# Kernel optimization log

Measured on AMD Instinct MI355X. Metric: run time of the kernel, lower is better.

The kernel has to match this reference:

```python
import jax, jax.numpy as jnp
import numpy as np

D_MODEL = 512
N_HEAD = 8
D_HEAD = D_MODEL // N_HEAD
NEG_INF = -1e30


def _rel_shift(x):
    # x: [b, h, i, j]  -- Transformer-XL relative shift trick
    b, h, i, j = x.shape
    x = jnp.pad(x, ((0, 0), (0, 0), (0, 0), (1, 0)))  # pad left on last dim
    x = x.reshape(b, h, j + 1, i)[:, :, 1:, :]
    return x.reshape(b, h, i, j)


def setup_inputs() -> dict:
    key = jax.random.key(0)
    ks = jax.random.split(key, 12)
    b, s = 2, 2048
    inp = {
        "q_in": jax.random.normal(ks[0], (b, s, D_MODEL), jnp.float32),
        "k_in": jax.random.normal(ks[1], (b, s, D_MODEL), jnp.float32),
        "v_in": jax.random.normal(ks[2], (b, s, D_MODEL), jnp.float32),
        "rel_r": jax.random.normal(ks[3], (s, D_MODEL), jnp.float32),
        "rel_u": jax.random.normal(ks[4], (N_HEAD, D_HEAD), jnp.float32) * 0.02,
        "rel_v": jax.random.normal(ks[5], (N_HEAD, D_HEAD), jnp.float32) * 0.02,
        "attn_mask": jnp.triu(jnp.ones((s, s), dtype=bool), k=1),  # causal: True = masked
        # learned params ([out, in] like torch Linear)
        "Wq": jax.random.normal(ks[6], (D_MODEL, D_MODEL), jnp.float32) * (D_MODEL ** -0.5),
        "Wk": jax.random.normal(ks[7], (D_MODEL, D_MODEL), jnp.float32) * (D_MODEL ** -0.5),
        "Wv": jax.random.normal(ks[8], (D_MODEL, D_MODEL), jnp.float32) * (D_MODEL ** -0.5),
        "Wr": jax.random.normal(ks[9], (D_MODEL, D_MODEL), jnp.float32) * (D_MODEL ** -0.5),
        "fc_w": jax.random.normal(ks[10], (D_MODEL, D_MODEL), jnp.float32) * (D_MODEL ** -0.5),
        "fc_b": jax.random.normal(ks[11], (D_MODEL,), jnp.float32) * 0.01,
    }
    return inp


def reference(q_in, k_in, v_in, rel_r, rel_u, rel_v, attn_mask,
              Wq, Wk, Wv, Wr, fc_w, fc_b):
    b, i, _ = q_in.shape
    j = k_in.shape[1]
    h, d = rel_u.shape
    scale = d ** -0.5

    q = (q_in @ Wq.T).reshape(b, i, h, d)
    k = (k_in @ Wk.T).reshape(b, j, h, d)
    v = (v_in @ Wv.T).reshape(b, j, h, d)
    r = (rel_r @ Wr.T).reshape(j, h, d)

    AC = jnp.einsum('bihd,bjhd->bhij', q + rel_u, k)
    BD = _rel_shift(jnp.einsum('bihd,jhd->bhij', q + rel_v, r))
    attn_score = (AC + BD) * scale

    attn_score = jnp.where(attn_mask[None, None, :, :], NEG_INF, attn_score)
    attn_prob = jax.nn.softmax(attn_score, axis=-1)

    attn_vec = jnp.einsum('bhij,bjhd->bihd', attn_prob, v).reshape(b, i, h * d)
    return attn_vec @ fc_w.T + fc_b
```

## Files before the change

### kernel.cpp

```cpp
#include <hip/hip_runtime.h>

typedef _Float16 half8 __attribute__((ext_vector_type(8)));
typedef float f32x4 __attribute__((ext_vector_type(4)));

constexpr int S    = 2048;
constexpr int DMO  = 512;
constexpr int NHD  = 8;
constexpr int DH   = 64;
constexpr int BB   = 2;
constexpr int RRROWS = 64 + S + 64;

constexpr size_t OFF_W  = 0;
constexpr size_t OFF_QU = OFF_W  + (size_t)5*512*512;
constexpr size_t OFF_QV = OFF_QU + (size_t)BB*NHD*S*DH;
constexpr size_t OFF_K  = OFF_QV + (size_t)BB*NHD*S*DH;
constexpr size_t OFF_V  = OFF_K  + (size_t)BB*NHD*S*DH;
constexpr size_t OFF_VT = OFF_V  + (size_t)BB*NHD*S*DH;
constexpr size_t OFF_RR = OFF_VT + (size_t)BB*NHD*S*DH;
constexpr size_t OFF_AV = OFF_RR + (size_t)NHD*RRROWS*DH;

static __device__ __forceinline__ f32x4 mfma16(half8 a, half8 b, f32x4 c) {
  return __builtin_amdgcn_mfma_f32_16x16x32_f16(a, b, c, 0, 0, 0);
}

__global__ __launch_bounds__(256) void k_convert(
    const float* __restrict__ Wq, const float* __restrict__ Wk,
    const float* __restrict__ Wv, const float* __restrict__ Wr,
    const float* __restrict__ fcw, _Float16* __restrict__ ws)
{
  const int idx = blockIdx.x * 256 + threadIdx.x;
  constexpr int WTOT = 5 * 512 * 512 / 4;
  if (idx < WTOT) {
    const int i4  = idx * 4;
    const int w   = i4 >> 18;
    const int off = i4 & (512 * 512 - 1);
    const float* src = (w == 0) ? Wq : (w == 1) ? Wk : (w == 2) ? Wv : (w == 3) ? Wr : fcw;
    const float4 v = *(const float4*)(src + off);
    _Float16* dst = ws + OFF_W + (size_t)w * 512 * 512 + off;
    dst[0] = (_Float16)v.x; dst[1] = (_Float16)v.y;
    dst[2] = (_Float16)v.z; dst[3] = (_Float16)v.w;
  } else {
    const int p = idx - WTOT;
    if (p < NHD * 128 * DH / 4) {
      const int e   = p * 4;
      const int h   = e >> 13;
      const int rem = e & 8191;
      const int rr  = rem >> 6;
      const int col = rem & 63;
      const int row = (rr < 64) ? rr : (2048 + rr);
      _Float16* dst = ws + OFF_RR + ((size_t)h * RRROWS + row) * DH + col;
      dst[0] = (_Float16)0.f; dst[1] = (_Float16)0.f;
      dst[2] = (_Float16)0.f; dst[3] = (_Float16)0.f;
    }
  }
}

__global__ __launch_bounds__(256, 4) void k_proj(
    const float* __restrict__ q_in, const float* __restrict__ k_in,
    const float* __restrict__ v_in, const float* __restrict__ rel_r,
    const float* __restrict__ rel_u, const float* __restrict__ rel_v,
    _Float16* __restrict__ ws)
{
  __shared__ _Float16 SM[64 * 72 + 128 * 72];
  _Float16* As = SM;
  _Float16* Bs = SM + 64 * 72;
  const int bid = blockIdx.x;
  int op, bx, by;
  if (bid < 768) { op = bid >> 8; const int t = bid & 255; bx = t & 63; by = t >> 6; }
  else           { op = 3;        const int t = bid - 768; bx = t & 31; by = t >> 5; }
  const int m0 = bx * 64, n0 = by * 128;
  const float*    Ap = (op == 0) ? q_in : (op == 1) ? k_in : (op == 2) ? v_in : rel_r;
  const _Float16* Bw = ws + OFF_W + (size_t)op * 512 * 512;

  const int tid  = threadIdx.x;
  const int lane = tid & 63, wv = tid >> 6;
  const int wm = wv >> 1, wn = wv & 1;
  const int lr = lane >> 4, lc = lane & 15;
  const int srowA = tid >> 2, skA = (tid & 3) * 16;
  const int srowB = tid >> 1, skB = (tid & 1) * 32;

  const float* Asrc = Ap + (size_t)(m0 + srowA) * 512 + skA;
  const _Float16* Bsrc = Bw + (size_t)(n0 + srowB) * 512 + skB;

  f32x4 acc[2][4];
#pragma unroll
  for (int i = 0; i < 2; ++i)
#pragma unroll
    for (int j = 0; j < 4; ++j) acc[i][j] = {0.f, 0.f, 0.f, 0.f};

  float4 apre[4];
  half8  bpre[4];
#pragma unroll
  for (int q = 0; q < 4; ++q) apre[q] = ((const float4*)Asrc)[q];
#pragma unroll
  for (int q = 0; q < 4; ++q) bpre[q] = *(const half8*)(Bsrc + q * 8);

  for (int kt = 0; kt < 8; ++kt) {
    {
      _Float16* d = As + srowA * 72 + skA;
#pragma unroll
      for (int q = 0; q < 2; ++q) {
        const float4 a = apre[2 * q];
        const float4 b = apre[2 * q + 1];
        half8 h;
        h[0] = (_Float16)a.x; h[1] = (_Float16)a.y; h[2] = (_Float16)a.z; h[3] = (_Float16)a.w;
        h[4] = (_Float16)b.x; h[5] = (_Float16)b.y; h[6] = (_Float16)b.z; h[7] = (_Float16)b.w;
        *(half8*)(d + q * 8) = h;
      }
      _Float16* db = Bs + srowB * 72 + skB;
#pragma unroll
      for (int q = 0; q < 4; ++q) *(half8*)(db + q * 8) = bpre[q];
    }
    __syncthreads();

    if (kt + 1 < 8) {
      const int k1 = (kt + 1) * 64;
#pragma unroll
      for (int q = 0; q < 4; ++q) apre[q] = ((const float4*)(Asrc + k1))[q];
#pragma unroll
      for (int q = 0; q < 4; ++q) bpre[q] = *(const half8*)(Bsrc + k1 + q * 8);
    }

    __builtin_amdgcn_s_setprio(1);
#pragma unroll
    for (int ks = 0; ks < 2; ++ks) {
      half8 a[2], b[4];
#pragma unroll
      for (int f = 0; f < 2; ++f)
        a[f] = *(const half8*)(As + (wm * 32 + f * 16 + lc) * 72 + ks * 32 + lr * 8);
#pragma unroll
      for (int f = 0; f < 4; ++f)
        b[f] = *(const half8*)(Bs + (wn * 64 + f * 16 + lc) * 72 + ks * 32 + lr * 8);
#pragma unroll
      for (int fm = 0; fm < 2; ++fm)
#pragma unroll
        for (int fn = 0; fn < 4; ++fn)
          acc[fm][fn] = mfma16(a[fm], b[fn], acc[fm][fn]);
    }
    __builtin_amdgcn_s_setprio(0);
    __syncthreads();
  }

  _Float16* Cs = SM;
#pragma unroll
  for (int fm = 0; fm < 2; ++fm)
#pragma unroll
    for (int fn = 0; fn < 4; ++fn)
#pragma unroll
      for (int r = 0; r < 4; ++r)
        Cs[(wm * 32 + fm * 16 + lr * 4 + r) * 140 + wn * 64 + fn * 16 + lc] =
            (_Float16)acc[fm][fn][r];
  __syncthreads();

  if (op == 2) {
    const int b = m0 >> 11, sbase = m0 & 2047;
    const int lcs = tid & 15;
#pragma unroll
    for (int q2 = 0; q2 < 4; ++q2) {
      const int c  = tid + q2 * 256;
      const int hs = c >> 9;
      const int rem = c & 511;
      const int d  = rem >> 3;
      const int s8 = (rem & 7) * 8;
      half8 hv;
#pragma unroll
      for (int i = 0; i < 8; ++i) {
        const int ii2 = (i + lcs) & 7;
        hv[ii2] = Cs[(s8 + ii2) * 140 + hs * 64 + d];
      }
      _Float16* dst = ws + OFF_VT + (size_t)(b * NHD + (n0 >> 6) + hs) * DH * S;
      *(half8*)(dst + (size_t)d * S + sbase + s8) = hv;
    }
    return;
  }

  const int row = tid >> 2;
  const int c32 = (tid & 3) * 32;
  const int m   = m0 + row;
  const int hh  = (n0 + c32) >> 6;
  const int dd  = c32 & 63;
  if (op == 0) {
    constexpr float SC = 0.125f * 1.44269504088896f;
    const int b = m >> 11, s = m & 2047;
    const size_t base = ((size_t)(b * NHD + hh) * S + s) * DH + dd;
#pragma unroll
    for (int q = 0; q < 4; ++q) {
      const half8 cv = *(const half8*)(Cs + row * 140 + c32 + q * 8);
      half8 ou, ov;
#pragma unroll
      for (int i = 0; i < 8; ++i) {
        const int n = n0 + c32 + q * 8 + i;
        const float v = (float)cv[i];
        ou[i] = (_Float16)((v + rel_u[n]) * SC);
        ov[i] = (_Float16)((v + rel_v[n]) * SC);
      }
      *(half8*)(ws + OFF_QU + base + q * 8) = ou;
      *(half8*)(ws + OFF_QV + base + q * 8) = ov;
    }
  } else if (op == 1) {
    const int b = m >> 11, s = m & 2047;
    _Float16* dst = ws + OFF_K + ((size_t)(b * NHD + hh) * S + s) * DH + dd;
#pragma unroll
    for (int q = 0; q < 4; ++q)
      *(half8*)(dst + q * 8) = *(const half8*)(Cs + row * 140 + c32 + q * 8);
  } else {
    const int rr = 2111 - m;
    _Float16* dst = ws + OFF_RR + ((size_t)hh * RRROWS + rr) * DH + dd;
#pragma unroll
    for (int q = 0; q < 4; ++q)
      *(half8*)(dst + q * 8) = *(const half8*)(Cs + row * 140 + c32 + q * 8);
  }
}

__global__ __launch_bounds__(256, 3) void k_attn(_Float16* __restrict__ ws)
{
  __shared__ _Float16 Ks[64 * 72];
  __shared__ _Float16 Vs[64 * 72];
  __shared__ _Float16 Rs[128 * 72];
  __shared__ _Float16 DsPs[64 * 88];

  const int bid = blockIdx.x;
  const int qi  = bid >> 5;
  const int qt  = 31 - qi;
  const int bh  = bid & 15;
  const int sp  = (bid >> 4) & 1;
  const int i0  = qt * 64;
  const int h   = bh & 7;

  const int nt = qt + 1;
  const int nh = (nt + 1) >> 1;
  const int jb = sp ? nh : 0;
  const int je = sp ? nt : nh;

  const _Float16* Qu = ws + OFF_QU + (size_t)bh * S * DH;
  const _Float16* Qv = ws + OFF_QV + (size_t)bh * S * DH;
  const _Float16* Kg = ws + OFF_K  + (size_t)bh * S * DH;
  const _Float16* VT = ws + OFF_VT + (size_t)bh * DH * S;
  const _Float16* RR = ws + OFF_RR + (size_t)h * RRROWS * DH;
  _Float16* PO = ws + (sp ? OFF_AV : OFF_V);
  float*    ML = (float*)ws;

  const int tid = threadIdx.x, lane = tid & 63, wv = tid >> 6;
  const int lr = lane >> 4, lc = lane & 15;

  half8 qu[2], qv[2];
  {
    const size_t ro = (size_t)(i0 + wv * 16 + lc) * DH + lr * 8;
    qu[0] = *(const half8*)(Qu + ro); qu[1] = *(const half8*)(Qu + ro + 32);
    qv[0] = *(const half8*)(Qv + ro); qv[1] = *(const half8*)(Qv + ro + 32);
  }

  f32x4 oacc[4];
#pragma unroll
  for (int i = 0; i < 4; ++i) oacc[i] = {0.f, 0.f, 0.f, 0.f};
  float lrow[4] = {0.f, 0.f, 0.f, 0.f};

  {
    const int j0 = jb * 64;
    const _Float16* src = Kg + (size_t)j0 * DH;
#pragma unroll
    for (int q = 0; q < 2; ++q) {
      const int c = tid + q * 256;
      *(half8*)(Ks + (c >> 3) * 72 + (c & 7) * 8) = *(const half8*)(src + c * 8);
    }
#pragma unroll
    for (int q = 0; q < 2; ++q) {
      const int c = tid + q * 256;
      const int d = c >> 3, cp = (c & 7) * 8;
      *(half8*)(Vs + d * 72 + cp) = *(const half8*)(VT + (size_t)d * S + j0 + cp);
    }
    const int r0 = i0 - j0 + 1;
#pragma unroll
    for (int q = 0; q < 4; ++q) {
      const int c = tid + q * 256;
      const int row = c >> 3, cp = (c & 7) * 8;
      const int a = r0 + row;
      *(half8*)(Rs + (a & 127) * 72 + cp) = *(const half8*)(RR + (size_t)a * DH + cp);
    }
  }
  __syncthreads();

  for (int jt = jb; jt < je; ++jt) {
    const int j0 = jt * 64;
    const int r0 = i0 - j0 + 1;

    {
      f32x4 dacc[5];
#pragma unroll
      for (int i = 0; i < 5; ++i) dacc[i] = {0.f, 0.f, 0.f, 0.f};
      __builtin_amdgcn_s_setprio(1);
#pragma unroll
      for (int cf = 0; cf < 5; ++cf)
#pragma unroll
        for (int ks = 0; ks < 2; ++ks) {
          const int prow = (r0 + (wv + cf) * 16 + lc) & 127;
          const half8 rb = *(const half8*)(Rs + prow * 72 + ks * 32 + lr * 8);
          dacc[cf] = mfma16(qv[ks], rb, dacc[cf]);
        }
      __builtin_amdgcn_s_setprio(0);
#pragma unroll
      for (int cf = 0; cf < 5; ++cf)
#pragma unroll
        for (int r = 0; r < 4; ++r)
          DsPs[(wv * 16 + lr * 4 + r) * 88 + cf * 16 + lc] = (_Float16)dacc[cf][r];
    }

    const bool more = (jt + 1 < je);
    half8 knx[2], vnx[2], rnx[2];
    if (more) {
      const int j1 = j0 + 64;
      const _Float16* srcK = Kg + (size_t)j1 * DH;
#pragma unroll
      for (int q = 0; q < 2; ++q) {
        const int c = tid + q * 256;
        knx[q] = *(const half8*)(srcK + c * 8);
      }
#pragma unroll
      for (int q = 0; q < 2; ++q) {
        const int c = tid + q * 256;
        const int d = c >> 3, cp = (c & 7) * 8;
        vnx[q] = *(const half8*)(VT + (size_t)d * S + j1 + cp);
      }
      const int r1 = r0 - 64;
#pragma unroll
      for (int q = 0; q < 2; ++q) {
        const int c = tid + q * 256;
        const int row = c >> 3, cp = (c & 7) * 8;
        rnx[q] = *(const half8*)(RR + (size_t)(r1 + row) * DH + cp);
      }
    }

    f32x4 sacc[4];
#pragma unroll
    for (int i = 0; i < 4; ++i) sacc[i] = {0.f, 0.f, 0.f, 0.f};
    __builtin_amdgcn_s_setprio(1);
#pragma unroll
    for (int jf = 0; jf < 4; ++jf)
#pragma unroll
      for (int ks = 0; ks < 2; ++ks) {
        const half8 kb = *(const half8*)(Ks + (jf * 16 + lc) * 72 + ks * 32 + lr * 8);
        sacc[jf] = mfma16(qu[ks], kb, sacc[jf]);
      }
    __builtin_amdgcn_s_setprio(0);

    const bool diag = (j0 == i0);
    float sv[4][4];
#pragma unroll
    for (int jf = 0; jf < 4; ++jf)
#pragma unroll
      for (int r = 0; r < 4; ++r) {
        const int rr4 = lr * 4 + r;
        const int ii  = wv * 16 + rr4;
        const int jj  = jf * 16 + lc;
        float x = sacc[jf][r] + (float)DsPs[ii * 88 + rr4 + 63 - jj];
        if (diag && (jj > ii)) x = -1e30f;
        sv[jf][r] = x;
      }

#pragma unroll
    for (int jf = 0; jf < 4; ++jf)
#pragma unroll
      for (int r = 0; r < 4; ++r) {
        const int ii = wv * 16 + lr * 4 + r;
        const int jj = jf * 16 + lc;
        const float p = exp2f(sv[jf][r] - 17.3123404906676f);
        lrow[r] += p;
        DsPs[ii * 88 + jj] = (_Float16)p;
      }

    __builtin_amdgcn_s_setprio(1);
#pragma unroll
    for (int ks = 0; ks < 2; ++ks) {
      const half8 pa = *(const half8*)(DsPs + (wv * 16 + lc) * 88 + ks * 32 + lr * 8);
#pragma unroll
      for (int nf = 0; nf < 4; ++nf) {
        const half8 vb = *(const half8*)(Vs + (nf * 16 + lc) * 72 + ks * 32 + lr * 8);
        oacc[nf] = mfma16(pa, vb, oacc[nf]);
      }
    }
    __builtin_amdgcn_s_setprio(0);

    if (more) {
      __syncthreads();
#pragma unroll
      for (int q = 0; q < 2; ++q) {
        const int c = tid + q * 256;
        *(half8*)(Ks + (c >> 3) * 72 + (c & 7) * 8) = knx[q];
      }
#pragma unroll
      for (int q = 0; q < 2; ++q) {
        const int c = tid + q * 256;
        const int d = c >> 3, cp = (c & 7) * 8;
        *(half8*)(Vs + d * 72 + cp) = vnx[q];
      }
      const int r1 = r0 - 64;
#pragma unroll
      for (int q = 0; q < 2; ++q) {
        const int c = tid + q * 256;
        const int row = c >> 3, cp = (c & 7) * 8;
        const int a = r1 + row;
        *(half8*)(Rs + (a & 127) * 72 + cp) = rnx[q];
      }
      __syncthreads();
    }
  }

#pragma unroll
  for (int r = 0; r < 4; ++r)
#pragma unroll
    for (int d = 1; d < 16; d <<= 1)
      lrow[r] += __shfl_xor(lrow[r], d);

#pragma unroll
  for (int nf = 0; nf < 4; ++nf)
#pragma unroll
    for (int r = 0; r < 4; ++r) {
      const int row = i0 + wv * 16 + lr * 4 + r;
      PO[((size_t)bh * S + row) * DH + nf * 16 + lc] = (_Float16)oacc[nf][r];
    }
  if (lc == 0) {
#pragma unroll
    for (int r = 0; r < 4; ++r) {
      const int row = i0 + wv * 16 + lr * 4 + r;
      const int idx = (sp * 16 + bh) * S + row;
      ML[65536 + idx] = lrow[r];
    }
  }
}

__global__ __launch_bounds__(256, 3) void k_fc(
    const _Float16* __restrict__ ws, const float* __restrict__ fc_b,
    float* __restrict__ out)
{
  __shared__ _Float16 As[64 * 72];
  __shared__ _Float16 Bs[64 * 72];
  const int m0 = blockIdx.x * 64, n0 = blockIdx.y * 64;
  const int tid = threadIdx.x;
  const int lane = tid & 63, wv = tid >> 6;
  const int wm = wv >> 1, wn = wv & 1;
  const int lr = lane >> 4, lc = lane & 15;
  const int srowA = tid >> 2, c4 = (tid & 3) * 16;
  const _Float16* PO0 = ws + OFF_V;
  const _Float16* PO1 = ws + OFF_AV;
  const float*    ML  = (const float*)ws;
  const _Float16* Bw  = ws + OFF_W + (size_t)4 * 512 * 512;

  const int am = m0 + srowA;
  const int ab = am >> 11, as = am & 2047;
  const _Float16* Bsrc = Bw + (size_t)(n0 + srowA) * 512 + c4;

  f32x4 acc[2][2];
#pragma unroll
  for (int i = 0; i < 2; ++i)
#pragma unroll
    for (int j = 0; j < 2; ++j) acc[i][j] = {0.f, 0.f, 0.f, 0.f};

  half8 p0pre[2], p1pre[2], bpre[2];
  float l0p, l1p;
  {
    const int bhA = ab * NHD;
    const int mlidx = bhA * S + as;
    l0p = ML[65536 + mlidx]; l1p = ML[65536 + 16 * 2048 + mlidx];
    const size_t base = ((size_t)bhA * S + as) * DH + c4;
#pragma unroll
    for (int q = 0; q < 2; ++q) {
      p0pre[q] = *(const half8*)(PO0 + base + q * 8);
      p1pre[q] = *(const half8*)(PO1 + base + q * 8);
      bpre[q]  = *(const half8*)(Bsrc + q * 8);
    }
  }

  for (int kt = 0; kt < 8; ++kt) {
    {
      const float inv = 1.f / (l0p + l1p);
      _Float16* d = As + srowA * 72 + c4;
#pragma unroll
      for (int q = 0; q < 2; ++q) {
        half8 o;
#pragma unroll
        for (int i = 0; i < 8; ++i)
          o[i] = (_Float16)(((float)p0pre[q][i] + (float)p1pre[q][i]) * inv);
        *(half8*)(d + q * 8) = o;
      }
      _Float16* db = Bs + srowA * 72 + c4;
#pragma unroll
      for (int q = 0; q < 2; ++q) *(half8*)(db + q * 8) = bpre[q];
    }
    __syncthreads();

    if (kt + 1 < 8) {
      const int bhA = ab * NHD + kt + 1;
      const int mlidx = bhA * S + as;
      l0p = ML[65536 + mlidx]; l1p = ML[65536 + 16 * 2048 + mlidx];
      const size_t base = ((size_t)bhA * S + as) * DH + c4;
#pragma unroll
      for (int q = 0; q < 2; ++q) {
        p0pre[q] = *(const half8*)(PO0 + base + q * 8);
        p1pre[q] = *(const half8*)(PO1 + base + q * 8);
        bpre[q]  = *(const half8*)(Bsrc + (kt + 1) * 64 + q * 8);
      }
    }

    __builtin_amdgcn_s_setprio(1);
#pragma unroll
    for (int ks = 0; ks < 2; ++ks) {
      half8 a[2], bfr[2];
#pragma unroll
      for (int f = 0; f < 2; ++f)
        a[f] = *(const half8*)(As + (wm * 32 + f * 16 + lc) * 72 + ks * 32 + lr * 8);
#pragma unroll
      for (int f = 0; f < 2; ++f)
        bfr[f] = *(const half8*)(Bs + (wn * 32 + f * 16 + lc) * 72 + ks * 32 + lr * 8);
#pragma unroll
      for (int fm = 0; fm < 2; ++fm)
#pragma unroll
        for (int fn = 0; fn < 2; ++fn)
          acc[fm][fn] = mfma16(a[fm], bfr[fn], acc[fm][fn]);
    }
    __builtin_amdgcn_s_setprio(0);
    __syncthreads();
  }
#pragma unroll
  for (int fm = 0; fm < 2; ++fm)
#pragma unroll
    for (int fn = 0; fn < 2; ++fn)
#pragma unroll
      for (int r = 0; r < 4; ++r) {
        const int m = m0 + wm * 32 + fm * 16 + lr * 4 + r;
        const int n = n0 + wn * 32 + fn * 16 + lc;
        out[(size_t)m * 512 + n] = acc[fm][fn][r] + fc_b[n];
      }
}

extern "C" void kernel_launch(void* const* d_in, const int* in_sizes, int n_in,
                              void* d_out, int out_size, void* d_ws, size_t ws_size,
                              hipStream_t stream)
{
  (void)in_sizes; (void)n_in; (void)out_size; (void)ws_size;
  const float* q_in  = (const float*)d_in[0];
  const float* k_in  = (const float*)d_in[1];
  const float* v_in  = (const float*)d_in[2];
  const float* rel_r = (const float*)d_in[3];
  const float* rel_u = (const float*)d_in[4];
  const float* rel_v = (const float*)d_in[5];
  const float* Wq   = (const float*)d_in[7];
  const float* Wk   = (const float*)d_in[8];
  const float* Wv   = (const float*)d_in[9];
  const float* Wr   = (const float*)d_in[10];
  const float* fc_w = (const float*)d_in[11];
  const float* fc_b = (const float*)d_in[12];
  _Float16* ws = (_Float16*)d_ws;
  float* out = (float*)d_out;

  k_convert<<<1344, 256, 0, stream>>>(Wq, Wk, Wv, Wr, fc_w, ws);
  k_proj<<<896, 256, 0, stream>>>(q_in, k_in, v_in, rel_r, rel_u, rel_v, ws);
  k_attn<<<1024, 256, 0, stream>>>(ws);
  dim3 gf(64, 8);
  k_fc<<<gf, 256, 0, stream>>>(ws, fc_b, out);
}
```

Before: 80.60 us.

## Enlarge attention query tile to 128 rows with 512-thread blocks

Each attention block now covers 128 query rows with eight waves instead of 64 rows with four, so every K, V and relative-position tile loaded into shared memory is reused by twice as many queries. The relative-position ring buffer grows to 192 rows with modulo indexing. The causal mask now applies to both key tiles that overlap the diagonal, and the grid shrinks to 512 blocks. In exchange, shared memory per block roughly doubles, which lowers occupancy, and there are fewer blocks to balance the triangular causal workload.

```diff
diff --git a/kernel.cpp b/kernel.cpp
--- a/kernel.cpp
+++ b/kernel.cpp
@@ -212,23 +212,22 @@
   }
 }
 
-__global__ __launch_bounds__(256, 3) void k_attn(_Float16* __restrict__ ws)
+__global__ __launch_bounds__(512, 4) void k_attn(_Float16* __restrict__ ws)
 {
   __shared__ _Float16 Ks[64 * 72];
   __shared__ _Float16 Vs[64 * 72];
-  __shared__ _Float16 Rs[128 * 72];
-  __shared__ _Float16 DsPs[64 * 88];
+  __shared__ _Float16 Rs[192 * 72];
+  __shared__ _Float16 DsPs[128 * 88];
 
   const int bid = blockIdx.x;
-  const int qi  = bid >> 5;
-  const int qt  = 31 - qi;
+  const int qt  = 15 - (bid >> 5);
   const int bh  = bid & 15;
   const int sp  = (bid >> 4) & 1;
-  const int i0  = qt * 64;
+  const int i0  = qt * 128;
   const int h   = bh & 7;
 
-  const int nt = qt + 1;
-  const int nh = (nt + 1) >> 1;
+  const int nt = 2 * qt + 2;
+  const int nh = qt + 1;
   const int jb = sp ? nh : 0;
   const int je = sp ? nt : nh;
 
@@ -258,24 +257,20 @@
   {
     const int j0 = jb * 64;
     const _Float16* src = Kg + (size_t)j0 * DH;
-#pragma unroll
-    for (int q = 0; q < 2; ++q) {
-      const int c = tid + q * 256;
+    {
+      const int c = tid;
       *(half8*)(Ks + (c >> 3) * 72 + (c & 7) * 8) = *(const half8*)(src + c * 8);
-    }
-#pragma unroll
-    for (int q = 0; q < 2; ++q) {
-      const int c = tid + q * 256;
       const int d = c >> 3, cp = (c & 7) * 8;
       *(half8*)(Vs + d * 72 + cp) = *(const half8*)(VT + (size_t)d * S + j0 + cp);
     }
     const int r0 = i0 - j0 + 1;
 #pragma unroll
-    for (int q = 0; q < 4; ++q) {
-      const int c = tid + q * 256;
+    for (int q = 0; q < 3; ++q) {
+      const int c = tid + q * 512;
       const int row = c >> 3, cp = (c & 7) * 8;
       const int a = r0 + row;
-      *(half8*)(Rs + (a & 127) * 72 + cp) = *(const half8*)(RR + (size_t)a * DH + cp);
+      const int phys = (a + 2304) % 192;
+      *(half8*)(Rs + phys * 72 + cp) = *(const half8*)(RR + (long)a * DH + cp);
     }
   }
   __syncthreads();
@@ -293,7 +288,7 @@
       for (int cf = 0; cf < 5; ++cf)
 #pragma unroll
         for (int ks = 0; ks < 2; ++ks) {
-          const int prow = (r0 + (wv + cf) * 16 + lc) & 127;
+          const int prow = (r0 + (wv + cf) * 16 + lc + 2304) % 192;
           const half8 rb = *(const half8*)(Rs + prow * 72 + ks * 32 + lr * 8);
           dacc[cf] = mfma16(qv[ks], rb, dacc[cf]);
         }
@@ -306,28 +301,16 @@
     }
 
     const bool more = (jt + 1 < je);
-    half8 knx[2], vnx[2], rnx[2];
+    half8 knx, vnx, rnx;
     if (more) {
       const int j1 = j0 + 64;
-      const _Float16* srcK = Kg + (size_t)j1 * DH;
-#pragma unroll
-      for (int q = 0; q < 2; ++q) {
-        const int c = tid + q * 256;
-        knx[q] = *(const half8*)(srcK + c * 8);
-      }
-#pragma unroll
-      for (int q = 0; q < 2; ++q) {
-        const int c = tid + q * 256;
-        const int d = c >> 3, cp = (c & 7) * 8;
-        vnx[q] = *(const half8*)(VT + (size_t)d * S + j1 + cp);
-      }
+      const int c = tid;
+      knx = *(const half8*)(Kg + (size_t)j1 * DH + c * 8);
+      const int d = c >> 3, cp = (c & 7) * 8;
+      vnx = *(const half8*)(VT + (size_t)d * S + j1 + cp);
       const int r1 = r0 - 64;
-#pragma unroll
-      for (int q = 0; q < 2; ++q) {
-        const int c = tid + q * 256;
-        const int row = c >> 3, cp = (c & 7) * 8;
-        rnx[q] = *(const half8*)(RR + (size_t)(r1 + row) * DH + cp);
-      }
+      const int row = c >> 3;
+      rnx = *(const half8*)(RR + (long)(r1 + row) * DH + cp);
     }
 
     f32x4 sacc[4];
@@ -343,7 +326,7 @@
       }
     __builtin_amdgcn_s_setprio(0);
 
-    const bool diag = (j0 == i0);
+    const bool nd = (j0 >= i0);
     float sv[4][4];
 #pragma unroll
     for (int jf = 0; jf < 4; ++jf)
@@ -353,7 +336,7 @@
         const int ii  = wv * 16 + rr4;
         const int jj  = jf * 16 + lc;
         float x = sacc[jf][r] + (float)DsPs[ii * 88 + rr4 + 63 - jj];
-        if (diag && (jj > ii)) x = -1e30f;
+        if (nd && (j0 + jj > i0 + ii)) x = -1e30f;
         sv[jf][r] = x;
       }
 
@@ -382,24 +365,15 @@
 
     if (more) {
       __syncthreads();
-#pragma unroll
-      for (int q = 0; q < 2; ++q) {
-        const int c = tid + q * 256;
-        *(half8*)(Ks + (c >> 3) * 72 + (c & 7) * 8) = knx[q];
-      }
-#pragma unroll
-      for (int q = 0; q < 2; ++q) {
-        const int c = tid + q * 256;
+      {
+        const int c = tid;
+        *(half8*)(Ks + (c >> 3) * 72 + (c & 7) * 8) = knx;
         const int d = c >> 3, cp = (c & 7) * 8;
-        *(half8*)(Vs + d * 72 + cp) = vnx[q];
-      }
-      const int r1 = r0 - 64;
-#pragma unroll
-      for (int q = 0; q < 2; ++q) {
-        const int c = tid + q * 256;
-        const int row = c >> 3, cp = (c & 7) * 8;
-        const int a = r1 + row;
-        *(half8*)(Rs + (a & 127) * 72 + cp) = rnx[q];
+        *(half8*)(Vs + d * 72 + cp) = vnx;
+        const int r1 = r0 - 64;
+        const int a = r1 + (c >> 3);
+        const int phys = (a + 2304) % 192;
+        *(half8*)(Rs + phys * 72 + cp) = rnx;
       }
       __syncthreads();
     }
@@ -554,7 +528,7 @@
 
   k_convert<<<1344, 256, 0, stream>>>(Wq, Wk, Wv, Wr, fc_w, ws);
   k_proj<<<896, 256, 0, stream>>>(q_in, k_in, v_in, rel_r, rel_u, rel_v, ws);
-  k_attn<<<1024, 256, 0, stream>>>(ws);
+  k_attn<<<512, 512, 0, stream>>>(ws);
   dim3 gf(64, 8);
   k_fc<<<gf, 256, 0, stream>>>(ws, fc_b, out);
 }
```

Result: slower. 89.25 us (+10.7%).
